# Optimization experiments

Hardware: AMD Instinct MI355X
Metric: run time of the kernel (lower is better)

The kernel has to match this reference:

```python
import jax, jax.numpy as jnp
import numpy as np

N = 8192            # number of candidate boxes (S*S*B proposals)
NUM_CLASSES = 80    # COCO
IOU_THRESHOLD = 0.5


def setup_inputs() -> dict:
    key = jax.random.key(0)
    k1, k2, k3, k4 = jax.random.split(key, 4)
    # valid boxes: x1,y1 in [0,500), w,h in [1,101) -> x2>x1, y2>y1
    xy = jax.random.uniform(k1, (N, 2), dtype=jnp.float32) * 500.0
    wh = jax.random.uniform(k2, (N, 2), dtype=jnp.float32) * 100.0 + 1.0
    obj = jax.random.uniform(k3, (N, 1), dtype=jnp.float32)
    cls = jax.random.uniform(k4, (N, NUM_CLASSES), dtype=jnp.float32)
    X = jnp.concatenate([xy, xy + wh, obj, cls], axis=1)  # (N, 5+C)
    return {"X": X}


def reference(X):
    """Faithful jax version of torchvision.ops.batched_nms applied to YOLO output.

    Returns X reordered by descending combined score, with suppressed rows
    zeroed (fixed output shape instead of data-dependent X[nms_idx]).
    """
    cls_probs = X[:, 5:]                       # (N, C)
    score = jnp.max(cls_probs, axis=1)         # per-box best class prob
    cat = jnp.argmax(cls_probs, axis=1)        # per-box class id
    scores = X[:, 4] * score                   # objectness * class prob

    boxes = X[:, 0:4]
    # batched_nms class-offset trick: shift boxes of different classes apart
    max_coord = jnp.max(boxes)
    offsets = cat.astype(boxes.dtype) * (max_coord + 1.0)
    b = boxes + offsets[:, None]               # (N, 4)

    order = jnp.argsort(-scores)               # descending score
    b = b[order]

    # pairwise IoU, (N, N)
    area = (b[:, 2] - b[:, 0]) * (b[:, 3] - b[:, 1])           # (N,)
    lt = jnp.maximum(b[:, None, :2], b[None, :, :2])           # (N,N,2)
    rb = jnp.minimum(b[:, None, 2:], b[None, :, 2:])           # (N,N,2)
    wh = jnp.clip(rb - lt, 0.0)
    inter = wh[..., 0] * wh[..., 1]
    iou = inter / (area[:, None] + area[None, :] - inter)

    n = b.shape[0]
    idx = jnp.arange(n)

    def body(i, supp):
        # if box i survives, suppress all later boxes overlapping it
        row = (iou[i] > IOU_THRESHOLD) & (idx > i) & jnp.logical_not(supp[i])
        return supp | row

    suppressed = jax.lax.fori_loop(0, n, body, jnp.zeros((n,), dtype=bool))
    keep = jnp.logical_not(suppressed)          # (N,) mask in score order

    return X[order] * keep[:, None].astype(X.dtype)
```

## Files before the change

kernel.cpp:

```cpp
#include <hip/hip_runtime.h>


#define N 8192
#define NC 80
#define COLS 85
#define MPC 192

__global__ __launch_bounds__(256) void score_kernel(const float* __restrict__ X,
                                                    unsigned long long* __restrict__ keys,
                                                    int* __restrict__ cat,
                                                    float* __restrict__ maxarr) {
    int wave = threadIdx.x >> 6;
    int lane = threadIdx.x & 63;
    int row = blockIdx.x * 4 + wave;
    const float* rp = X + (size_t)row * COLS;

    float v1 = rp[5 + lane];
    float v2 = (lane < 16) ? rp[5 + 64 + lane] : -INFINITY;
    float bv; int bi;
    if (v2 > v1) { bv = v2; bi = lane + 64; } else { bv = v1; bi = lane; }
    #pragma unroll
    for (int m = 32; m >= 1; m >>= 1) {
        float ov = __shfl_xor(bv, m, 64);
        int   oi = __shfl_xor(bi, m, 64);
        if (ov > bv || (ov == bv && oi < bi)) { bv = ov; bi = oi; }
    }
    float c = (lane < 4) ? rp[lane] : 0.0f;
    #pragma unroll
    for (int m = 32; m >= 1; m >>= 1) c = fmaxf(c, __shfl_xor(c, m, 64));

    __shared__ float cmax[4];
    if (lane == 0) {
        float s = __fmul_rn(rp[4], bv);
        keys[row] = ((unsigned long long)__float_as_uint(s) << 13)
                  | (unsigned long long)(8191 - row);
        cat[row] = bi;
        cmax[wave] = c;
    }
    __syncthreads();
    if (threadIdx.x == 0)
        maxarr[blockIdx.x] = fmaxf(fmaxf(cmax[0], cmax[1]), fmaxf(cmax[2], cmax[3]));
}

__global__ __launch_bounds__(1024) void rank_kernel(const unsigned long long* __restrict__ keys,
                                                    int* __restrict__ rank) {
    __shared__ unsigned long long ikey[32];
    __shared__ int part[32 * 17];

    const int t    = threadIdx.x;
    const int wave = t >> 6;
    const int lane = t & 63;

    unsigned long long key[8];
    #pragma unroll
    for (int k = 0; k < 8; ++k) key[k] = keys[t + 1024 * k];
    if (t < 32) ikey[t] = keys[blockIdx.x * 32 + t];
    __syncthreads();

    unsigned long long Ki = ikey[0];
    for (int ii = 0; ii < 32; ++ii) {
        unsigned long long Kn = ikey[(ii + 1) & 31];
        int cnt = 0;
        #pragma unroll
        for (int k = 0; k < 8; ++k)
            cnt += __popcll(__ballot(key[k] > Ki));
        if (lane == 0) part[ii * 17 + wave] = cnt;
        Ki = Kn;
    }
    __syncthreads();
    if (t < 32) {
        int g = 0;
        #pragma unroll
        for (int w = 0; w < 16; ++w) g += part[t * 17 + w];
        rank[blockIdx.x * 32 + t] = g;
    }
}

__global__ __launch_bounds__(1024) void nms_out_kernel(const float* __restrict__ X,
                                                       const unsigned long long* __restrict__ keys,
                                                       const int* __restrict__ cat,
                                                       const int* __restrict__ rank,
                                                       const float* __restrict__ maxarr,
                                                       float* __restrict__ out) {
    __shared__ unsigned long long mkey[MPC];
    __shared__ int           mj[MPC];
    __shared__ float4        lbox[MPC];
    __shared__ float         larea[MPC];
    __shared__ int           lrow[MPC];
    __shared__ int           lorig[MPC];
    __shared__ unsigned long long Pm[MPC][3];
    __shared__ unsigned char lkeep[MPC];
    __shared__ float         swmax[16];
    __shared__ int           mcount;

    const int t    = threadIdx.x;
    const int wave = t >> 6;
    const int lane = t & 63;
    const int c    = blockIdx.x;

    if (t == 0) mcount = 0;

    float tm = fmaxf(maxarr[t], maxarr[t + 1024]);
    #pragma unroll
    for (int m = 32; m >= 1; m >>= 1) tm = fmaxf(tm, __shfl_xor(tm, m, 64));
    if (lane == 0) swmax[wave] = tm;
    __syncthreads();
    float gmax = swmax[0];
    #pragma unroll
    for (int w = 1; w < 16; ++w) gmax = fmaxf(gmax, swmax[w]);
    const float F = __fadd_rn(gmax, 1.0f);

    #pragma unroll
    for (int k = 0; k < 8; ++k) {
        int j = t + 1024 * k;
        if (cat[j] == c) {
            int pos = atomicAdd(&mcount, 1);
            if (pos < MPC) { mkey[pos] = keys[j]; mj[pos] = j; }
        }
    }
    __syncthreads();
    int M = mcount < MPC ? mcount : MPC;
    if (M == 0) return;

    if (t < M) {
        unsigned long long Kt = mkey[t];
        int cr = 0;
        #pragma unroll 4
        for (int m2 = 0; m2 < M; ++m2) cr += (int)(mkey[m2] > Kt);
        int orig = mj[t];
        int g = rank[orig];
        const float* rp = X + (size_t)orig * COLS;
        float off = __fmul_rn((float)c, F);
        float b0 = __fadd_rn(rp[0], off);
        float b1 = __fadd_rn(rp[1], off);
        float b2 = __fadd_rn(rp[2], off);
        float b3 = __fadd_rn(rp[3], off);
        lbox[cr]  = make_float4(b0, b1, b2, b3);
        larea[cr] = __fmul_rn(__fsub_rn(b2, b0), __fsub_rn(b3, b1));
        lrow[cr]  = g;
        lorig[cr] = orig;
    }
    __syncthreads();

    float4 mbox[3]; float marea[3];
    #pragma unroll
    for (int s = 0; s < 3; ++s) {
        int j = (s << 6) + lane;
        if (j < M) { mbox[s] = lbox[j]; marea[s] = larea[j]; }
        else       { mbox[s] = make_float4(0.f, 0.f, 0.f, 0.f); marea[s] = 0.f; }
    }

    for (int i = wave; i < M; i += 16) {
        float4 cb = lbox[i];
        float  ca = larea[i];
        unsigned long long w0, w1, w2;
        #pragma unroll
        for (int s = 0; s < 3; ++s) {
            int j = (s << 6) + lane;
            int pred = 0;
            if (j > i && j < M) {
                float ltx = fmaxf(cb.x, mbox[s].x), lty = fmaxf(cb.y, mbox[s].y);
                float rbx = fminf(cb.z, mbox[s].z), rby = fminf(cb.w, mbox[s].w);
                float wx = fmaxf(__fsub_rn(rbx, ltx), 0.0f);
                float wy = fmaxf(__fsub_rn(rby, lty), 0.0f);
                float inter = __fmul_rn(wx, wy);
                float denom = __fsub_rn(__fadd_rn(ca, marea[s]), inter);
                float iou = __fdiv_rn(inter, denom);
                pred = (iou > 0.5f) ? 1 : 0;
            }
            unsigned long long bm = __ballot(pred);
            if (s == 0) w0 = bm; else if (s == 1) w1 = bm; else w2 = bm;
        }
        if (lane == 0) { Pm[i][0] = w0; Pm[i][1] = w1; Pm[i][2] = w2; }
    }
    __syncthreads();

    if (t < 64) {
        unsigned long long r0 = 0, r1 = 0, r2 = 0;
        unsigned long long p0 = Pm[0][0], p1 = Pm[0][1], p2 = Pm[0][2];
        #pragma unroll 4
        for (int i = 0; i < M; ++i) {
            int ip = (i + 1 < M) ? i + 1 : i;
            unsigned long long q0 = Pm[ip][0], q1 = Pm[ip][1], q2 = Pm[ip][2];
            unsigned long long cur = (i < 64) ? r0 : ((i < 128) ? r1 : r2);
            if (((cur >> (i & 63)) & 1ULL) == 0ULL) {
                r0 |= p0; r1 |= p1; r2 |= p2;
            }
            p0 = q0; p1 = q1; p2 = q2;
        }
        if (lane < M)       lkeep[lane]       = (unsigned char)((r0 >> lane) & 1ULL);
        if (64 + lane < M)  lkeep[64 + lane]  = (unsigned char)((r1 >> lane) & 1ULL);
        if (128 + lane < M) lkeep[128 + lane] = (unsigned char)((r2 >> lane) & 1ULL);
    }
    __syncthreads();

    for (int m = wave; m < M; m += 16) {
        float keepf = lkeep[m] ? 0.0f : 1.0f;
        const float* src = X + (size_t)lorig[m] * COLS;
        float*       dst = out + (size_t)lrow[m] * COLS;
        float v0 = src[lane];
        float v1 = (lane < COLS - 64) ? src[64 + lane] : 0.0f;
        dst[lane] = __fmul_rn(v0, keepf);
        if (lane < COLS - 64) dst[64 + lane] = __fmul_rn(v1, keepf);
    }
}

extern "C" void kernel_launch(void* const* d_in, const int* in_sizes, int n_in,
                              void* d_out, int out_size, void* d_ws, size_t ws_size,
                              hipStream_t stream) {
    const float* X = (const float*)d_in[0];
    float* out = (float*)d_out;
    char* ws = (char*)d_ws;

    unsigned long long* keys = (unsigned long long*)(ws + 0);
    int*   cat    = (int*)(ws + 65536);
    float* maxarr = (float*)(ws + 98304);
    int*   rank   = (int*)(ws + 106496);

    score_kernel<<<N / 4, 256, 0, stream>>>(X, keys, cat, maxarr);
    rank_kernel<<<N / 32, 1024, 0, stream>>>(keys, rank);
    nms_out_kernel<<<NC, 1024, 0, stream>>>(X, keys, cat, rank, maxarr, out);
}
```

Measured before the change: 90.17 us.

## Scatter boxes per class in rank kernel and split output copy into flat kernel

The rank kernel now also computes the class offset and appends each box, with its rank and original index, into per-class buckets through global atomics. This removes the per-class scan over all 8192 category entries and the O(M^2) in-class rank loop from the NMS kernel. In-class order now comes from a bitmap and prefix-popcount over global ranks. The NMS kernel writes a compact keep/origin map, and a new fully parallel kernel does the gather-multiply output copy instead of 80 blocks copying rows. The cost is one extra kernel launch and extra workspace traffic.

After: 95.10 us. 1.05x slower.

```diff
diff --git a/kernel.cpp b/kernel.cpp
--- a/kernel.cpp
+++ b/kernel.cpp
@@ -9,7 +9,10 @@
 __global__ __launch_bounds__(256) void score_kernel(const float* __restrict__ X,
                                                     unsigned long long* __restrict__ keys,
                                                     int* __restrict__ cat,
-                                                    float* __restrict__ maxarr) {
+                                                    float* __restrict__ maxarr,
+                                                    int* __restrict__ ccount) {
+    if (blockIdx.x == 0 && threadIdx.x < NC) ccount[threadIdx.x] = 0;
+
     int wave = threadIdx.x >> 6;
     int lane = threadIdx.x & 63;
     int row = blockIdx.x * 4 + wave;
@@ -42,20 +45,41 @@
         maxarr[blockIdx.x] = fmaxf(fmaxf(cmax[0], cmax[1]), fmaxf(cmax[2], cmax[3]));
 }
 
-__global__ __launch_bounds__(1024) void rank_kernel(const unsigned long long* __restrict__ keys,
-                                                    int* __restrict__ rank) {
+__global__ __launch_bounds__(1024) void rank_scatter_kernel(
+        const float* __restrict__ X,
+        const unsigned long long* __restrict__ keys,
+        const int* __restrict__ cat,
+        const float* __restrict__ maxarr,
+        int* __restrict__ ccount,
+        float4* __restrict__ cbox,
+        float* __restrict__ carea,
+        int* __restrict__ cg,
+        int* __restrict__ corig) {
     __shared__ unsigned long long ikey[32];
-    __shared__ int part[32 * 17];
+    __shared__ int   icat[32];
+    __shared__ int   part[32 * 17];
+    __shared__ float swmax[16];
 
     const int t    = threadIdx.x;
     const int wave = t >> 6;
     const int lane = t & 63;
+    const int base = blockIdx.x * 32;
+
+    float tm = fmaxf(maxarr[t], maxarr[t + 1024]);
+    #pragma unroll
+    for (int m = 32; m >= 1; m >>= 1) tm = fmaxf(tm, __shfl_xor(tm, m, 64));
+    if (lane == 0) swmax[wave] = tm;
 
     unsigned long long key[8];
     #pragma unroll
     for (int k = 0; k < 8; ++k) key[k] = keys[t + 1024 * k];
-    if (t < 32) ikey[t] = keys[blockIdx.x * 32 + t];
-    __syncthreads();
+    if (t < 32) { ikey[t] = keys[base + t]; icat[t] = cat[base + t]; }
+    __syncthreads();
+
+    float gmax = swmax[0];
+    #pragma unroll
+    for (int w = 1; w < 16; ++w) gmax = fmaxf(gmax, swmax[w]);
+    const float F = __fadd_rn(gmax, 1.0f);
 
     unsigned long long Ki = ikey[0];
     for (int ii = 0; ii < 32; ++ii) {
@@ -68,75 +92,86 @@
         Ki = Kn;
     }
     __syncthreads();
+
     if (t < 32) {
         int g = 0;
         #pragma unroll
         for (int w = 0; w < 16; ++w) g += part[t * 17 + w];
-        rank[blockIdx.x * 32 + t] = g;
-    }
-}
-
-__global__ __launch_bounds__(1024) void nms_out_kernel(const float* __restrict__ X,
-                                                       const unsigned long long* __restrict__ keys,
-                                                       const int* __restrict__ cat,
-                                                       const int* __restrict__ rank,
-                                                       const float* __restrict__ maxarr,
-                                                       float* __restrict__ out) {
-    __shared__ unsigned long long mkey[MPC];
-    __shared__ int           mj[MPC];
+        int i  = base + t;
+        int ci = icat[t];
+        int slot = atomicAdd(&ccount[ci], 1);
+        if (slot < MPC) {
+            const float* rp = X + (size_t)i * COLS;
+            float off = __fmul_rn((float)ci, F);
+            float b0 = __fadd_rn(rp[0], off);
+            float b1 = __fadd_rn(rp[1], off);
+            float b2 = __fadd_rn(rp[2], off);
+            float b3 = __fadd_rn(rp[3], off);
+            int p = ci * MPC + slot;
+            cbox[p]  = make_float4(b0, b1, b2, b3);
+            carea[p] = __fmul_rn(__fsub_rn(b2, b0), __fsub_rn(b3, b1));
+            cg[p]    = g;
+            corig[p] = i;
+        }
+    }
+}
+
+__global__ __launch_bounds__(1024) void nms_kernel(const float4* __restrict__ cbox,
+                                                   const float* __restrict__ carea,
+                                                   const int* __restrict__ cg,
+                                                   const int* __restrict__ corig,
+                                                   const int* __restrict__ ccount,
+                                                   unsigned int* __restrict__ kmap) {
+    __shared__ unsigned long long bits[128];
+    __shared__ int           pfx[128];
     __shared__ float4        lbox[MPC];
     __shared__ float         larea[MPC];
     __shared__ int           lrow[MPC];
     __shared__ int           lorig[MPC];
     __shared__ unsigned long long Pm[MPC][3];
     __shared__ unsigned char lkeep[MPC];
-    __shared__ float         swmax[16];
-    __shared__ int           mcount;
 
     const int t    = threadIdx.x;
     const int wave = t >> 6;
     const int lane = t & 63;
     const int c    = blockIdx.x;
 
-    if (t == 0) mcount = 0;
-
-    float tm = fmaxf(maxarr[t], maxarr[t + 1024]);
-    #pragma unroll
-    for (int m = 32; m >= 1; m >>= 1) tm = fmaxf(tm, __shfl_xor(tm, m, 64));
-    if (lane == 0) swmax[wave] = tm;
-    __syncthreads();
-    float gmax = swmax[0];
-    #pragma unroll
-    for (int w = 1; w < 16; ++w) gmax = fmaxf(gmax, swmax[w]);
-    const float F = __fadd_rn(gmax, 1.0f);
-
-    #pragma unroll
-    for (int k = 0; k < 8; ++k) {
-        int j = t + 1024 * k;
-        if (cat[j] == c) {
-            int pos = atomicAdd(&mcount, 1);
-            if (pos < MPC) { mkey[pos] = keys[j]; mj[pos] = j; }
-        }
-    }
-    __syncthreads();
-    int M = mcount < MPC ? mcount : MPC;
+    int M = ccount[c];
+    if (M > MPC) M = MPC;
     if (M == 0) return;
 
+    if (t < 128) bits[t] = 0ULL;
+
+    float4 b; float a; int g = 0, orig = 0;
     if (t < M) {
-        unsigned long long Kt = mkey[t];
-        int cr = 0;
-        #pragma unroll 4
-        for (int m2 = 0; m2 < M; ++m2) cr += (int)(mkey[m2] > Kt);
-        int orig = mj[t];
-        int g = rank[orig];
-        const float* rp = X + (size_t)orig * COLS;
-        float off = __fmul_rn((float)c, F);
-        float b0 = __fadd_rn(rp[0], off);
-        float b1 = __fadd_rn(rp[1], off);
-        float b2 = __fadd_rn(rp[2], off);
-        float b3 = __fadd_rn(rp[3], off);
-        lbox[cr]  = make_float4(b0, b1, b2, b3);
-        larea[cr] = __fmul_rn(__fsub_rn(b2, b0), __fsub_rn(b3, b1));
+        int p = c * MPC + t;
+        b = cbox[p]; a = carea[p]; g = cg[p]; orig = corig[p];
+    }
+    __syncthreads();
+    if (t < M) atomicOr(&bits[g >> 6], 1ULL << (g & 63));
+    __syncthreads();
+
+    if (t < 64) {
+        int s0 = (int)__popcll(bits[lane]);
+        int s1 = (int)__popcll(bits[64 + lane]);
+        int x0 = s0, x1 = s1;
+        #pragma unroll
+        for (int d = 1; d < 64; d <<= 1) {
+            int v0 = __shfl_up(x0, d, 64);
+            int v1 = __shfl_up(x1, d, 64);
+            if (lane >= d) { x0 += v0; x1 += v1; }
+        }
+        int tot0 = __shfl(x0, 63, 64);
+        pfx[lane]      = x0 - s0;
+        pfx[64 + lane] = x1 - s1 + tot0;
+    }
+    __syncthreads();
+
+    if (t < M) {
+        int w = g >> 6;
+        int cr = pfx[w] + (int)__popcll(bits[w] & ((1ULL << (g & 63)) - 1ULL));
+        lbox[cr]  = b;
+        larea[cr] = a;
         lrow[cr]  = g;
         lorig[cr] = orig;
     }
@@ -194,15 +229,19 @@
     }
     __syncthreads();
 
-    for (int m = wave; m < M; m += 16) {
-        float keepf = lkeep[m] ? 0.0f : 1.0f;
-        const float* src = X + (size_t)lorig[m] * COLS;
-        float*       dst = out + (size_t)lrow[m] * COLS;
-        float v0 = src[lane];
-        float v1 = (lane < COLS - 64) ? src[64 + lane] : 0.0f;
-        dst[lane] = __fmul_rn(v0, keepf);
-        if (lane < COLS - 64) dst[64 + lane] = __fmul_rn(v1, keepf);
-    }
+    if (t < M)
+        kmap[lrow[t]] = (unsigned int)lorig[t] | (lkeep[t] ? 0x80000000u : 0u);
+}
+
+__global__ __launch_bounds__(1024) void out_kernel(const float* __restrict__ X,
+                                                   const unsigned int* __restrict__ kmap,
+                                                   float* __restrict__ out) {
+    int idx = blockIdx.x * 1024 + threadIdx.x;
+    int r = idx / COLS;
+    int col = idx - r * COLS;
+    unsigned int v = kmap[r];
+    float f = (v & 0x80000000u) ? 0.0f : 1.0f;
+    out[idx] = __fmul_rn(X[(size_t)(v & 0x1FFFu) * COLS + col], f);
 }
 
 extern "C" void kernel_launch(void* const* d_in, const int* in_sizes, int n_in,
@@ -213,11 +252,18 @@
     char* ws = (char*)d_ws;
 
     unsigned long long* keys = (unsigned long long*)(ws + 0);
-    int*   cat    = (int*)(ws + 65536);
-    float* maxarr = (float*)(ws + 98304);
-    int*   rank   = (int*)(ws + 106496);
-
-    score_kernel<<<N / 4, 256, 0, stream>>>(X, keys, cat, maxarr);
-    rank_kernel<<<N / 32, 1024, 0, stream>>>(keys, rank);
-    nms_out_kernel<<<NC, 1024, 0, stream>>>(X, keys, cat, rank, maxarr, out);
-}
+    int*          cat    = (int*)(ws + 65536);
+    float*        maxarr = (float*)(ws + 98304);
+    int*          ccount = (int*)(ws + 106496);
+    unsigned int* kmap   = (unsigned int*)(ws + 110592);
+    float4*       cbox   = (float4*)(ws + 147456);
+    float*        carea  = (float*)(ws + 393216);
+    int*          cg     = (int*)(ws + 454656);
+    int*          corig  = (int*)(ws + 516096);
+
+    score_kernel<<<N / 4, 256, 0, stream>>>(X, keys, cat, maxarr, ccount);
+    rank_scatter_kernel<<<N / 32, 1024, 0, stream>>>(X, keys, cat, maxarr, ccount,
+                                                     cbox, carea, cg, corig);
+    nms_kernel<<<NC, 1024, 0, stream>>>(cbox, carea, cg, corig, ccount, kmap);
+    out_kernel<<<(N * COLS) / 1024, 1024, 0, stream>>>(X, kmap, out);
+}
```

## Fuse global rank computation into per-class NMS kernel, drop rank kernel

Applied to the files above, without the earlier changes.

Removes the separate rank kernel and computes each box's global rank inside the per-class NMS block, by ballot-counting all 8192 keys against that class's members eight keys at a time. Local order within the class is then derived from a bitmap of global ranks plus a prefix scan, instead of an O(M^2) shared-memory compare. Compaction now uses wave-aggregated atomics, and the serial suppression scan reads rows through register shuffles instead of LDS loads. The intent is to save a kernel launch and its global round trip. The cost is that only 80 blocks now do the ranking work, and each iterates over roughly 100+ class members.

Measured after the change: 113.3 us. 1.26x slower.

```diff
diff --git a/kernel.cpp b/kernel.cpp
--- a/kernel.cpp
+++ b/kernel.cpp
@@ -42,48 +42,17 @@
         maxarr[blockIdx.x] = fmaxf(fmaxf(cmax[0], cmax[1]), fmaxf(cmax[2], cmax[3]));
 }
 
-__global__ __launch_bounds__(1024) void rank_kernel(const unsigned long long* __restrict__ keys,
-                                                    int* __restrict__ rank) {
-    __shared__ unsigned long long ikey[32];
-    __shared__ int part[32 * 17];
-
-    const int t    = threadIdx.x;
-    const int wave = t >> 6;
-    const int lane = t & 63;
-
-    unsigned long long key[8];
-    #pragma unroll
-    for (int k = 0; k < 8; ++k) key[k] = keys[t + 1024 * k];
-    if (t < 32) ikey[t] = keys[blockIdx.x * 32 + t];
-    __syncthreads();
-
-    unsigned long long Ki = ikey[0];
-    for (int ii = 0; ii < 32; ++ii) {
-        unsigned long long Kn = ikey[(ii + 1) & 31];
-        int cnt = 0;
-        #pragma unroll
-        for (int k = 0; k < 8; ++k)
-            cnt += __popcll(__ballot(key[k] > Ki));
-        if (lane == 0) part[ii * 17 + wave] = cnt;
-        Ki = Kn;
-    }
-    __syncthreads();
-    if (t < 32) {
-        int g = 0;
-        #pragma unroll
-        for (int w = 0; w < 16; ++w) g += part[t * 17 + w];
-        rank[blockIdx.x * 32 + t] = g;
-    }
-}
-
-__global__ __launch_bounds__(1024) void nms_out_kernel(const float* __restrict__ X,
-                                                       const unsigned long long* __restrict__ keys,
-                                                       const int* __restrict__ cat,
-                                                       const int* __restrict__ rank,
-                                                       const float* __restrict__ maxarr,
-                                                       float* __restrict__ out) {
-    __shared__ unsigned long long mkey[MPC];
-    __shared__ int           mj[MPC];
+__global__ __launch_bounds__(1024) void nms_kernel(const float* __restrict__ X,
+                                                   const unsigned long long* __restrict__ keys,
+                                                   const int* __restrict__ cat,
+                                                   const float* __restrict__ maxarr,
+                                                   float* __restrict__ out) {
+    __shared__ unsigned long long mkeyU[MPC];
+    __shared__ int           mrow[MPC];
+    __shared__ int           mg[MPC];
+    __shared__ int           part[MPC * 17];
+    __shared__ unsigned long long bits[128];
+    __shared__ int           pfx[128];
     __shared__ float4        lbox[MPC];
     __shared__ float         larea[MPC];
     __shared__ int           lrow[MPC];
@@ -99,13 +68,23 @@
     const int c    = blockIdx.x;
 
     if (t == 0) mcount = 0;
+    if (t < 128) bits[t] = 0ULL;
 
     float tm = fmaxf(maxarr[t], maxarr[t + 1024]);
     #pragma unroll
     for (int m = 32; m >= 1; m >>= 1) tm = fmaxf(tm, __shfl_xor(tm, m, 64));
     if (lane == 0) swmax[wave] = tm;
-    __syncthreads();
-    float gmax = swmax[0];
+
+    unsigned long long key[8];
+    #pragma unroll
+    for (int k = 0; k < 8; ++k) key[k] = keys[t + 1024 * k];
+
+    int cat8[8];
+    #pragma unroll
+    for (int k = 0; k < 8; ++k) cat8[k] = cat[t + 1024 * k];
+    __syncthreads();
+    const float gmax0 = swmax[0];
+    float gmax = gmax0;
     #pragma unroll
     for (int w = 1; w < 16; ++w) gmax = fmaxf(gmax, swmax[w]);
     const float F = __fadd_rn(gmax, 1.0f);
@@ -113,22 +92,86 @@
     #pragma unroll
     for (int k = 0; k < 8; ++k) {
         int j = t + 1024 * k;
-        if (cat[j] == c) {
-            int pos = atomicAdd(&mcount, 1);
-            if (pos < MPC) { mkey[pos] = keys[j]; mj[pos] = j; }
+        int pred = (cat8[k] == c);
+        unsigned long long bm = __ballot(pred);
+        int npop = __popcll(bm);
+        int old = 0;
+        if (lane == 0 && npop) old = atomicAdd(&mcount, npop);
+        old = __shfl(old, 0, 64);
+        if (pred) {
+            int pos = old + __popcll(bm & ((1ULL << lane) - 1ULL));
+            if (pos < MPC) { mkeyU[pos] = key[k]; mrow[pos] = j; }
         }
     }
     __syncthreads();
     int M = mcount < MPC ? mcount : MPC;
     if (M == 0) return;
 
+    for (int mb = 0; mb < M; mb += 8) {
+        unsigned long long K0 = mkeyU[(mb + 0 < M) ? mb + 0 : M - 1];
+        unsigned long long K1 = mkeyU[(mb + 1 < M) ? mb + 1 : M - 1];
+        unsigned long long K2 = mkeyU[(mb + 2 < M) ? mb + 2 : M - 1];
+        unsigned long long K3 = mkeyU[(mb + 3 < M) ? mb + 3 : M - 1];
+        unsigned long long K4 = mkeyU[(mb + 4 < M) ? mb + 4 : M - 1];
+        unsigned long long K5 = mkeyU[(mb + 5 < M) ? mb + 5 : M - 1];
+        unsigned long long K6 = mkeyU[(mb + 6 < M) ? mb + 6 : M - 1];
+        unsigned long long K7 = mkeyU[(mb + 7 < M) ? mb + 7 : M - 1];
+        int c0 = 0, c1 = 0, c2 = 0, c3 = 0, c4 = 0, c5 = 0, c6 = 0, c7 = 0;
+        #pragma unroll
+        for (int k = 0; k < 8; ++k) {
+            unsigned long long kk = key[k];
+            c0 += __popcll(__ballot(kk > K0));
+            c1 += __popcll(__ballot(kk > K1));
+            c2 += __popcll(__ballot(kk > K2));
+            c3 += __popcll(__ballot(kk > K3));
+            c4 += __popcll(__ballot(kk > K4));
+            c5 += __popcll(__ballot(kk > K5));
+            c6 += __popcll(__ballot(kk > K6));
+            c7 += __popcll(__ballot(kk > K7));
+        }
+        if (lane == 0) {
+            if (mb + 0 < M) part[(mb + 0) * 17 + wave] = c0;
+            if (mb + 1 < M) part[(mb + 1) * 17 + wave] = c1;
+            if (mb + 2 < M) part[(mb + 2) * 17 + wave] = c2;
+            if (mb + 3 < M) part[(mb + 3) * 17 + wave] = c3;
+            if (mb + 4 < M) part[(mb + 4) * 17 + wave] = c4;
+            if (mb + 5 < M) part[(mb + 5) * 17 + wave] = c5;
+            if (mb + 6 < M) part[(mb + 6) * 17 + wave] = c6;
+            if (mb + 7 < M) part[(mb + 7) * 17 + wave] = c7;
+        }
+    }
+    __syncthreads();
+
     if (t < M) {
-        unsigned long long Kt = mkey[t];
-        int cr = 0;
-        #pragma unroll 4
-        for (int m2 = 0; m2 < M; ++m2) cr += (int)(mkey[m2] > Kt);
-        int orig = mj[t];
-        int g = rank[orig];
+        int g = 0;
+        #pragma unroll
+        for (int w = 0; w < 16; ++w) g += part[t * 17 + w];
+        mg[t] = g;
+        atomicOr(&bits[g >> 6], 1ULL << (g & 63));
+    }
+    __syncthreads();
+
+    if (t < 64) {
+        int s0 = (int)__popcll(bits[lane]);
+        int s1 = (int)__popcll(bits[64 + lane]);
+        int x0 = s0, x1 = s1;
+        #pragma unroll
+        for (int d = 1; d < 64; d <<= 1) {
+            int v0 = __shfl_up(x0, d, 64);
+            int v1 = __shfl_up(x1, d, 64);
+            if (lane >= d) { x0 += v0; x1 += v1; }
+        }
+        int tot0 = __shfl(x0, 63, 64);
+        pfx[lane]      = x0 - s0;
+        pfx[64 + lane] = x1 - s1 + tot0;
+    }
+    __syncthreads();
+
+    if (t < M) {
+        int g = mg[t];
+        int w = g >> 6;
+        int cr = pfx[w] + (int)__popcll(bits[w] & ((1ULL << (g & 63)) - 1ULL));
+        int orig = mrow[t];
         const float* rp = X + (size_t)orig * COLS;
         float off = __fmul_rn((float)c, F);
         float b0 = __fadd_rn(rp[0], off);
@@ -176,17 +219,20 @@
     __syncthreads();
 
     if (t < 64) {
+        unsigned long long h00 = Pm[lane][0],       h01 = Pm[lane][1],       h02 = Pm[lane][2];
+        unsigned long long h10 = Pm[64 + lane][0],  h11 = Pm[64 + lane][1],  h12 = Pm[64 + lane][2];
+        unsigned long long h20 = Pm[128 + lane][0], h21 = Pm[128 + lane][1], h22 = Pm[128 + lane][2];
         unsigned long long r0 = 0, r1 = 0, r2 = 0;
-        unsigned long long p0 = Pm[0][0], p1 = Pm[0][1], p2 = Pm[0][2];
-        #pragma unroll 4
         for (int i = 0; i < M; ++i) {
-            int ip = (i + 1 < M) ? i + 1 : i;
-            unsigned long long q0 = Pm[ip][0], q1 = Pm[ip][1], q2 = Pm[ip][2];
-            unsigned long long cur = (i < 64) ? r0 : ((i < 128) ? r1 : r2);
-            if (((cur >> (i & 63)) & 1ULL) == 0ULL) {
+            int slot = i >> 6;
+            int owner = i & 63;
+            unsigned long long p0, p1, p2, cur;
+            if (slot == 0)      { p0 = __shfl(h00, owner, 64); p1 = __shfl(h01, owner, 64); p2 = __shfl(h02, owner, 64); cur = r0; }
+            else if (slot == 1) { p0 = __shfl(h10, owner, 64); p1 = __shfl(h11, owner, 64); p2 = __shfl(h12, owner, 64); cur = r1; }
+            else                { p0 = __shfl(h20, owner, 64); p1 = __shfl(h21, owner, 64); p2 = __shfl(h22, owner, 64); cur = r2; }
+            if (((cur >> owner) & 1ULL) == 0ULL) {
                 r0 |= p0; r1 |= p1; r2 |= p2;
             }
-            p0 = q0; p1 = q1; p2 = q2;
         }
         if (lane < M)       lkeep[lane]       = (unsigned char)((r0 >> lane) & 1ULL);
         if (64 + lane < M)  lkeep[64 + lane]  = (unsigned char)((r1 >> lane) & 1ULL);
@@ -215,9 +261,7 @@
     unsigned long long* keys = (unsigned long long*)(ws + 0);
     int*   cat    = (int*)(ws + 65536);
     float* maxarr = (float*)(ws + 98304);
-    int*   rank   = (int*)(ws + 106496);
 
     score_kernel<<<N / 4, 256, 0, stream>>>(X, keys, cat, maxarr);
-    rank_kernel<<<N / 32, 1024, 0, stream>>>(keys, rank);
-    nms_out_kernel<<<NC, 1024, 0, stream>>>(X, keys, cat, rank, maxarr, out);
+    nms_kernel<<<NC, 1024, 0, stream>>>(X, keys, cat, maxarr, out);
 }
```

## Replace per-class key compare loop with rank bitmap and prefix-sum ordering

Applied to the files above, without the earlier changes.

In the per-class NMS kernel, the local order of the class members is no longer found by an O(M^2) comparison of 64-bit keys. Each member instead sets its global rank bit in a shared 8192-bit bitmap, and a wave-level prefix popcount over the bitmap gives each member its position within the class. Member collection now uses one ballot-aggregated atomic per wave instead of one atomic per thread, and the cat loads are hoisted ahead of the barrier. This adds two extra block barriers and a scan, and it no longer reads keys in this kernel.

Measured after the change: 86.95 us. 1.04x faster.

```diff
diff --git a/kernel.cpp b/kernel.cpp
--- a/kernel.cpp
+++ b/kernel.cpp
@@ -77,13 +77,13 @@
 }
 
 __global__ __launch_bounds__(1024) void nms_out_kernel(const float* __restrict__ X,
-                                                       const unsigned long long* __restrict__ keys,
                                                        const int* __restrict__ cat,
                                                        const int* __restrict__ rank,
                                                        const float* __restrict__ maxarr,
                                                        float* __restrict__ out) {
-    __shared__ unsigned long long mkey[MPC];
-    __shared__ int           mj[MPC];
+    __shared__ int           mrow[MPC];
+    __shared__ unsigned long long bits[128];
+    __shared__ int           pfx[128];
     __shared__ float4        lbox[MPC];
     __shared__ float         larea[MPC];
     __shared__ int           lrow[MPC];
@@ -99,11 +99,16 @@
     const int c    = blockIdx.x;
 
     if (t == 0) mcount = 0;
+    if (t < 128) bits[t] = 0ULL;
 
     float tm = fmaxf(maxarr[t], maxarr[t + 1024]);
     #pragma unroll
     for (int m = 32; m >= 1; m >>= 1) tm = fmaxf(tm, __shfl_xor(tm, m, 64));
     if (lane == 0) swmax[wave] = tm;
+
+    int cat8[8];
+    #pragma unroll
+    for (int k = 0; k < 8; ++k) cat8[k] = cat[t + 1024 * k];
     __syncthreads();
     float gmax = swmax[0];
     #pragma unroll
@@ -113,22 +118,47 @@
     #pragma unroll
     for (int k = 0; k < 8; ++k) {
         int j = t + 1024 * k;
-        if (cat[j] == c) {
-            int pos = atomicAdd(&mcount, 1);
-            if (pos < MPC) { mkey[pos] = keys[j]; mj[pos] = j; }
+        int pred = (cat8[k] == c);
+        unsigned long long bm = __ballot(pred);
+        int old = 0;
+        if (lane == 0 && bm) old = atomicAdd(&mcount, __popcll(bm));
+        old = __shfl(old, 0, 64);
+        if (pred) {
+            int pos = old + __popcll(bm & ((1ULL << lane) - 1ULL));
+            if (pos < MPC) mrow[pos] = j;
         }
     }
     __syncthreads();
     int M = mcount < MPC ? mcount : MPC;
     if (M == 0) return;
 
+    int g = 0, orig = 0;
     if (t < M) {
-        unsigned long long Kt = mkey[t];
-        int cr = 0;
-        #pragma unroll 4
-        for (int m2 = 0; m2 < M; ++m2) cr += (int)(mkey[m2] > Kt);
-        int orig = mj[t];
-        int g = rank[orig];
+        orig = mrow[t];
+        g = rank[orig];
+        atomicOr(&bits[g >> 6], 1ULL << (g & 63));
+    }
+    __syncthreads();
+
+    if (t < 64) {
+        int s0 = (int)__popcll(bits[lane]);
+        int s1 = (int)__popcll(bits[64 + lane]);
+        int x0 = s0, x1 = s1;
+        #pragma unroll
+        for (int d = 1; d < 64; d <<= 1) {
+            int v0 = __shfl_up(x0, d, 64);
+            int v1 = __shfl_up(x1, d, 64);
+            if (lane >= d) { x0 += v0; x1 += v1; }
+        }
+        int tot0 = __shfl(x0, 63, 64);
+        pfx[lane]      = x0 - s0;
+        pfx[64 + lane] = x1 - s1 + tot0;
+    }
+    __syncthreads();
+
+    if (t < M) {
+        int w = g >> 6;
+        int cr = pfx[w] + (int)__popcll(bits[w] & ((1ULL << (g & 63)) - 1ULL));
         const float* rp = X + (size_t)orig * COLS;
         float off = __fmul_rn((float)c, F);
         float b0 = __fadd_rn(rp[0], off);
@@ -219,5 +249,5 @@
 
     score_kernel<<<N / 4, 256, 0, stream>>>(X, keys, cat, maxarr);
     rank_kernel<<<N / 32, 1024, 0, stream>>>(keys, rank);
-    nms_out_kernel<<<NC, 1024, 0, stream>>>(X, keys, cat, rank, maxarr, out);
-}
+    nms_out_kernel<<<NC, 1024, 0, stream>>>(X, cat, rank, maxarr, out);
+}
```
